# Performance work log

Hardware: AMD Instinct MI355X
Metric: run time of the kernel (lower is better)

## Reference

```python
import jax, jax.numpy as jnp
import numpy as np

# TriangleMixConfig constants (from init_kwargs)
NUM_SINK_TOKENS = 4
SLIDING_WINDOW_SIZE = 32
NUM_LAST_TOKENS = 64


def setup_inputs() -> dict:
    return {"seq_len": 8192, "use_triangle": 1}


def _triangle_mask(seq_len: int) -> jnp.ndarray:
    """Vectorized Streaming + Last (Triangle) boolean mask, [N, N]."""
    si = NUM_SINK_TOKENS
    sl = SLIDING_WINDOW_SIZE
    last = NUM_LAST_TOKens if False else NUM_LAST_TOKENS
    i = jnp.arange(seq_len)[:, None]   # query index
    j = jnp.arange(seq_len)[None, :]   # key index
    causal = i >= j
    # Streaming: causal and (sink or within sliding window)
    streaming = causal & ((j <= si) | ((i - j) <= sl))
    # Last Q-K: causal, query in final `last` rows, key outside sink+window
    last_qk = causal & ((seq_len - i) < last) & (j > si) & ((i - j) > sl)
    return streaming | last_qk


def reference(seq_len, use_triangle):
    if use_triangle:
        mask = _triangle_mask(seq_len)
    else:
        i = jnp.arange(seq_len)[:, None]
        j = jnp.arange(seq_len)[None, :]
        mask = i >= j  # dense causal
    # allowed positions -> 0.0, disallowed -> -inf
    return jnp.where(mask, jnp.float32(0.0), jnp.float32(-jnp.inf))
```

## Files before the change

kernel.cpp:

```cpp
#include <hip/hip_runtime.h>
#include <math.h>

#define SINK   4
#define SLIDE  32
#define LAST   64

#define NEGBITS 0xFF7F0000u

__global__ __launch_bounds__(256) void triangle_mask_kernel(
        float* __restrict__ out,
        const int* __restrict__ use_tri_p,
        int N) {
    const int i  = blockIdx.y;
    const int j0 = (blockIdx.x * blockDim.x + threadIdx.x) * 4;
    if (j0 >= N) return;

    const int ut = *use_tri_p;
    const float NEGVAL = __uint_as_float(NEGBITS);

    const bool last_row = (N - i) < LAST;

    float v[4];
#pragma unroll
    for (int k = 0; k < 4; ++k) {
        const int j = j0 + k;
        const bool causal = (i >= j);
        const bool allow = ut
            ? (causal && ((j <= SINK) || ((i - j) <= SLIDE) || last_row))
            : causal;
        v[k] = allow ? 0.0f : NEGVAL;
    }

    if (j0 + 3 < N) {
        float4* outv = (float4*)(out + (size_t)i * N + j0);
        *outv = make_float4(v[0], v[1], v[2], v[3]);
    } else {
        for (int k = 0; k < 4 && (j0 + k) < N; ++k)
            out[(size_t)i * N + j0 + k] = v[k];
    }
}

extern "C" void kernel_launch(void* const* d_in, const int* in_sizes, int n_in,
                              void* d_out, int out_size, void* d_ws, size_t ws_size,
                              hipStream_t stream) {
    const int* use_tri = (const int*)d_in[1];

    const int N = (int)(sqrt((double)out_size) + 0.5);

    dim3 block(256);
    dim3 grid((unsigned)((N / 4 + 255) / 256), (unsigned)N);
    triangle_mask_kernel<<<grid, block, 0, stream>>>((float*)d_out, use_tri, N);
}
```

Measured before the change: 247.9 us.

## Use flat grid-stride loop with nontemporal vector stores for power-of-two N

Replaces the 2D grid of one row per block-row with a 1D grid-stride loop capped at 2048 blocks. For power-of-two N, row and column come from shift and mask, and each thread writes a 16-byte vector with a nontemporal store to avoid polluting the cache on this write-only 256 MB output. A scalar generic fallback is kept for other sizes, and it may be slower than the old kernel. The capped grid trades some parallelism for less launch and scheduling overhead.

```diff
diff --git a/kernel.cpp b/kernel.cpp
--- a/kernel.cpp
+++ b/kernel.cpp
@@ -7,36 +7,50 @@
 
 #define NEGBITS 0xFF7F0000u
 
-__global__ __launch_bounds__(256) void triangle_mask_kernel(
+typedef float f32x4 __attribute__((ext_vector_type(4)));
+
+__global__ __launch_bounds__(256) void triangle_mask_pow2(
+        float* __restrict__ out,
+        const int* __restrict__ use_tri_p,
+        int N, int sh , unsigned total4) {
+    const int ut = *use_tri_p;
+    const float NEGVAL = __uint_as_float(NEGBITS);
+    const unsigned stride = gridDim.x * blockDim.x;
+    const unsigned mask4 = (1u << sh) - 1u;
+
+    for (unsigned idx = blockIdx.x * blockDim.x + threadIdx.x;
+         idx < total4; idx += stride) {
+        const int i  = (int)(idx >> sh);
+        const int j0 = (int)((idx & mask4) << 2);
+        const bool open = (ut == 0) || ((N - i) < LAST);
+        f32x4 v;
+#pragma unroll
+        for (int k = 0; k < 4; ++k) {
+            const int j = j0 + k;
+            const bool allow = (i >= j) &&
+                (open || (j <= SINK) || ((i - j) <= SLIDE));
+            v[k] = allow ? 0.0f : NEGVAL;
+        }
+        __builtin_nontemporal_store(v, ((f32x4*)out) + idx);
+    }
+}
+
+__global__ __launch_bounds__(256) void triangle_mask_generic(
         float* __restrict__ out,
         const int* __restrict__ use_tri_p,
         int N) {
-    const int i  = blockIdx.y;
-    const int j0 = (blockIdx.x * blockDim.x + threadIdx.x) * 4;
-    if (j0 >= N) return;
-
     const int ut = *use_tri_p;
     const float NEGVAL = __uint_as_float(NEGBITS);
-
-    const bool last_row = (N - i) < LAST;
-
-    float v[4];
-#pragma unroll
-    for (int k = 0; k < 4; ++k) {
-        const int j = j0 + k;
-        const bool causal = (i >= j);
-        const bool allow = ut
-            ? (causal && ((j <= SINK) || ((i - j) <= SLIDE) || last_row))
-            : causal;
-        v[k] = allow ? 0.0f : NEGVAL;
-    }
-
-    if (j0 + 3 < N) {
-        float4* outv = (float4*)(out + (size_t)i * N + j0);
-        *outv = make_float4(v[0], v[1], v[2], v[3]);
-    } else {
-        for (int k = 0; k < 4 && (j0 + k) < N; ++k)
-            out[(size_t)i * N + j0 + k] = v[k];
+    const size_t total = (size_t)N * N;
+    const size_t stride = (size_t)gridDim.x * blockDim.x;
+    for (size_t idx = (size_t)blockIdx.x * blockDim.x + threadIdx.x;
+         idx < total; idx += stride) {
+        const int i = (int)(idx / (unsigned)N);
+        const int j = (int)(idx - (size_t)i * N);
+        const bool open = (ut == 0) || ((N - i) < LAST);
+        const bool allow = (i >= j) &&
+            (open || (j <= SINK) || ((i - j) <= SLIDE));
+        out[idx] = allow ? 0.0f : NEGVAL;
     }
 }
 
@@ -47,7 +61,19 @@
 
     const int N = (int)(sqrt((double)out_size) + 0.5);
 
-    dim3 block(256);
-    dim3 grid((unsigned)((N / 4 + 255) / 256), (unsigned)N);
-    triangle_mask_kernel<<<grid, block, 0, stream>>>((float*)d_out, use_tri, N);
+    if ((N & 3) == 0 && (N & (N - 1)) == 0) {
+        int sh = 0;
+        while ((1 << sh) != (N >> 2)) ++sh;
+        const unsigned total4 = (unsigned)(((size_t)N * N) >> 2);
+        unsigned blocks = (total4 + 255u) / 256u;
+        if (blocks > 2048u) blocks = 2048u;
+        triangle_mask_pow2<<<dim3(blocks), dim3(256), 0, stream>>>(
+            (float*)d_out, use_tri, N, sh, total4);
+    } else {
+        const size_t total = (size_t)N * N;
+        unsigned blocks = (unsigned)((total + 255u) / 256u);
+        if (blocks > 2048u) blocks = 2048u;
+        triangle_mask_generic<<<dim3(blocks), dim3(256), 0, stream>>>(
+            (float*)d_out, use_tri, N);
+    }
 }
```

After: 276.0 us. 1.11x slower.
